# Performance work log

Measured on AMD Instinct MI355X. Metric: run time of the kernel, lower is better.

## Reference

```python
import jax, jax.numpy as jnp
import numpy as np

N = 648      # code length (input_size = output_size)
DV = 3       # variable degree
DC = 6       # check degree
M_PER = N // DC            # checks per layer = 108
E = N * DV                 # edges = hidden_size = 1944
BATCH = 2048
CLAMP = 0.999999


def _build_graph():
    rng = np.random.default_rng(0)
    # regular (3,6) Tanner graph via 3 permutation layers
    var_of = np.concatenate([rng.permutation(N) for _ in range(DV)])          # [E]
    chk_of = np.repeat(np.arange(DV * M_PER), DC)                              # [E]
    eye = np.eye(E, dtype=bool)
    same_chk = (chk_of[:, None] == chk_of[None, :]) & ~eye                     # extrinsic same-check
    same_var = (var_of[:, None] == var_of[None, :]) & ~eye                     # extrinsic same-var
    M_ev = np.zeros((E, N), dtype=np.float32)
    M_ev[np.arange(E), var_of] = 1.0                                           # edge -> its variable
    M_first = (same_chk.astype(np.float32) @ M_ev)                             # [E,N] CN extrinsic over vars
    M_cn = same_chk.astype(np.float32)                                         # [E,E] VN2CN_mask_CNUpdate
    M_vn = same_var.astype(np.float32)                                         # [E,E] CN2VN_mask_VNUpdate
    M_out = M_ev.T.copy()                                                      # [N,E] CN2VN_mask_output
    bias_matrix = M_ev.T.copy()                                                # [N,E] dot_bias_matrix
    return M_first, M_cn, M_vn, M_out, bias_matrix


def _xavier(key, out_f, in_f, mask):
    bound = np.sqrt(6.0 / (in_f + out_f)).astype(np.float32)
    w = jax.random.uniform(key, (out_f, in_f), jnp.float32, -bound, bound)
    return w * mask


def setup_inputs() -> dict:
    key = jax.random.key(0)
    M_first, M_cn, M_vn, M_out, bias_matrix = _build_graph()
    M_first = jnp.asarray(M_first); M_cn = jnp.asarray(M_cn)
    M_vn = jnp.asarray(M_vn); M_out = jnp.asarray(M_out)
    bias_matrix = jnp.asarray(bias_matrix)
    ks = jax.random.split(key, 6)
    x = jax.random.normal(ks[0], (BATCH, N), jnp.float32) * 2.0  # channel LLRs
    W1 = _xavier(ks[1], E, E, M_vn)
    W3 = _xavier(ks[2], E, E, M_vn)
    W5 = _xavier(ks[3], E, E, M_vn)
    W7 = _xavier(ks[4], E, E, M_vn)
    W9 = _xavier(ks[5], N, E, M_out)
    B0 = jnp.eye(N, dtype=jnp.float32); B1 = jnp.eye(N, dtype=jnp.float32)
    B2 = jnp.eye(N, dtype=jnp.float32); B3 = jnp.eye(N, dtype=jnp.float32)
    B4 = jnp.eye(N, dtype=jnp.float32)
    return {"x": x, "M_first": M_first, "M_cn": M_cn, "M_out": M_out,
            "bias_matrix": bias_matrix, "W1": W1, "W3": W3, "W5": W5,
            "W7": W7, "W9": W9, "B0": B0, "B1": B1, "B2": B2, "B3": B3, "B4": B4}


def cn_update(x, mask):
    """out[b,i] = prod over j with mask[i,j]!=0 and x[b,j]!=0 of x[b,j]; 0 if none.
    Computed in sign/log domain so it is three dense [B,in]@[in,out] matmuls
    instead of a Python loop over rows."""
    nz = x != 0.0
    logmag = jnp.log(jnp.where(nz, jnp.abs(x), 1.0))          # 0 contribution where x==0
    neg = (x < 0.0).astype(x.dtype)
    log_prod = logmag @ mask.T                                 # [B,out]
    neg_cnt = neg @ mask.T
    sign = 1.0 - 2.0 * jnp.mod(neg_cnt, 2.0)
    any_nz = (nz.astype(x.dtype) @ mask.T) > 0.0
    return jnp.where(any_nz, sign * jnp.exp(log_prod), 0.0)


def reference(x, M_first, M_cn, M_out, bias_matrix, W1, W3, W5, W7, W9,
              B0, B1, B2, B3, B4):
    llr = x                                                    # Channel_LLR [B,N]
    t = jnp.tanh(0.5 * x)
    t = jnp.clip(cn_update(t, M_first), -CLAMP, CLAMP)
    t = 2.0 * jnp.arctanh(t)
    out1 = jax.nn.sigmoid(t @ M_out.T + llr)                   # count_loss_fc: ones*mask weight, zero bias

    t = jnp.tanh(0.5 * (t @ W1.T + (llr @ B0) @ bias_matrix))
    t = jnp.clip(cn_update(t, M_cn), -CLAMP, CLAMP)
    t = 2.0 * jnp.arctanh(t)
    out2 = jax.nn.sigmoid(t @ M_out.T + llr)

    t = jnp.tanh(0.5 * (t @ W3.T + (llr @ B1) @ bias_matrix))
    t = jnp.clip(cn_update(t, M_cn), -CLAMP, CLAMP)
    t = 2.0 * jnp.arctanh(t)
    out3 = jax.nn.sigmoid(t @ M_out.T + llr)

    t = jnp.tanh(0.5 * (t @ W5.T + (llr @ B2) @ bias_matrix))
    t = jnp.clip(cn_update(t, M_cn), -CLAMP, CLAMP)
    t = 2.0 * jnp.arctanh(t)
    out4 = jax.nn.sigmoid(t @ M_out.T + llr)

    t = jnp.tanh(0.5 * (t @ W7.T + (llr @ B3) @ bias_matrix))
    t = jnp.clip(cn_update(t, M_cn), -CLAMP, CLAMP)
    t = 2.0 * jnp.arctanh(t)
    t = t @ W9.T + llr @ B4
    out5 = jax.nn.sigmoid(t)
    return (out5, out4, out3, out2, out1)
```

## Files before the change

kernel.cpp:

```cpp
#include <hip/hip_runtime.h>
#include <math.h>

#define NN 648
#define EE 1944
#define NCHK 324
#define BATCH 2048
#define BS 256
#define BSM 384
#define TL_CLAMP 14.508648f

__device__ __forceinline__ float rcp_fast(float x) { return __builtin_amdgcn_rcpf(x); }

__device__ __forceinline__ float tanh_half(float x) {
    float E = __expf(x);
    float big = 1.0f - 2.0f * rcp_fast(E + 1.0f);
    float u = 0.5f * x;
    float small = u * (1.0f - 0.33333334f * u * u);
    return (fabsf(x) < 0.03125f) ? small : big;
}

__device__ __forceinline__ float sigm(float s) {
    return rcp_fast(1.0f + __expf(-s));
}

__device__ __forceinline__ float cn_edge(float a, float Q) {
    float t = 0.6931472f * (__log2f(fabsf(a + Q)) - __log2f(fabsf(a - Q)));
    return fminf(fmaxf(t, -TL_CLAMP), TL_CLAMP);
}

__device__ __noinline__ float cn_fallback(float a, float t0, float t1, float t2,
                                          float t3, float t4, float t5) {
    float vv[6] = {t0, t1, t2, t3, t4, t5};
    float P = 1.0f; int cz = 0;
    #pragma unroll
    for (int k = 0; k < 6; k++) {
        if (vv[k] == 0.0f) cz++; else P *= vv[k];
    }
    float ext;
    if (a != 0.0f) ext = (cz >= 5) ? 0.0f : P * rcp_fast(a);
    else           ext = (cz >= 6) ? 0.0f : P;
    ext = fminf(fmaxf(ext, -0.999999f), 0.999999f);
    return 0.6931472f * __log2f((1.0f + ext) * rcp_fast(1.0f - ext));
}

__global__ __launch_bounds__(BS) void extract_struct(
    const float4* __restrict__ M_out4,
    int* __restrict__ var_of, int* __restrict__ varEdge,
    unsigned short* __restrict__ varc16) {
    int t = blockIdx.x * BS + threadIdx.x;
    if (t >= NN * EE / 4) return;
    float4 v = M_out4[t];
    int flat = t * 4;
    int n = flat / EE;
    int e = flat - n * EE;
    if (v.x != 0.0f) { var_of[e]     = n; varEdge[n*3 + (e)    /NN] = e;     varc16[e]     = (unsigned short)n; }
    if (v.y != 0.0f) { var_of[e + 1] = n; varEdge[n*3 + (e + 1)/NN] = e + 1; varc16[e + 1] = (unsigned short)n; }
    if (v.z != 0.0f) { var_of[e + 2] = n; varEdge[n*3 + (e + 2)/NN] = e + 2; varc16[e + 2] = (unsigned short)n; }
    if (v.w != 0.0f) { var_of[e + 3] = n; varEdge[n*3 + (e + 3)/NN] = e + 3; varc16[e + 3] = (unsigned short)n; }
}

__global__ __launch_bounds__(BS) void extract_weights(
    const float* __restrict__ W1, const float* __restrict__ W3,
    const float* __restrict__ W5, const float* __restrict__ W7,
    const float* __restrict__ W9,
    const int* __restrict__ var_of, const int* __restrict__ varEdge,
    unsigned* __restrict__ nb6,
    float4* __restrict__ w1q, float4* __restrict__ w3q,
    float4* __restrict__ w5q, float4* __restrict__ w7q,
    float* __restrict__ w9v) {
    int t = blockIdx.x * BS + threadIdx.x;
    if (t < 4 * EE) {
        int m = t / EE;
        int e = t - m * EE;
        int n = var_of[e];
        int e0 = varEdge[3 * n], e1 = varEdge[3 * n + 1], e2 = varEdge[3 * n + 2];
        int ea, eb;
        if (e == e0)      { ea = e1; eb = e2; }
        else if (e == e1) { ea = e0; eb = e2; }
        else              { ea = e0; eb = e1; }
        const float* W = (m == 0) ? W1 : (m == 1) ? W3 : (m == 2) ? W5 : W7;
        size_t row = (size_t)e * EE;
        float2 w = make_float2(W[row + ea], W[row + eb]);
        float4* dq = (m == 0) ? w1q : (m == 1) ? w3q : (m == 2) ? w5q : w7q;
        ((float2*)dq)[e] = w;
        if (m == 0) nb6[e] = (unsigned)ea | ((unsigned)eb << 16);
    } else if (t < 4 * EE + NN) {
        int n = t - 4 * EE;
        #pragma unroll
        for (int k = 0; k < 3; k++) {
            int e = varEdge[3 * n + k];
            w9v[3 * n + k] = W9[(size_t)n * EE + e];
        }
    }
}

__global__ __launch_bounds__(BSM, 8) void bp_main(
    const float* __restrict__ x,
    const unsigned* __restrict__ varc,
    const unsigned* __restrict__ nb6,
    const int* __restrict__ varEdge,
    const float4* __restrict__ w1q, const float4* __restrict__ w3q,
    const float4* __restrict__ w5q, const float4* __restrict__ w7q,
    const float* __restrict__ w9v,
    float* __restrict__ out) {
    __shared__ __align__(16) float llr_s[NN];
    __shared__ __align__(16) float tlA[EE];
    __shared__ __align__(16) float tlB[EE];
    const int b = blockIdx.x;
    const int tid = threadIdx.x;

    {
        const float2* xr2 = (const float2*)(x + (size_t)b * NN);
        if (tid < NN / 2) ((float2*)llr_s)[tid] = xr2[tid];
    }
    __syncthreads();

    const bool ck = tid < NCHK;
    const int c = tid;
    float lb[6];
    unsigned nbp[6];
    float te[6];

    if (ck) {
        #pragma unroll
        for (int j = 0; j < 3; j++) {
            unsigned vv = varc[3 * c + j];
            lb[2 * j]     = llr_s[vv & 0xffffu];
            lb[2 * j + 1] = llr_s[vv >> 16];
        }
        #pragma unroll
        for (int j = 0; j < 6; j++) {
            nbp[j] = nb6[6 * c + j];
            te[j] = tanh_half(lb[j]);
        }
    }
    int m0[2], m1[2], m2[2];
    #pragma unroll
    for (int j = 0; j < 2; j++) {
        int n = tid + j * BSM;
        if (n < NN) {
            m0[j] = varEdge[3 * n]; m1[j] = varEdge[3 * n + 1];
            m2[j] = varEdge[3 * n + 2];
        } else { m0[j] = m1[j] = m2[j] = 0; }
    }

    auto cn_store = [&](float* dst) {
        float Q = ((te[0] * te[1]) * (te[2] * te[3])) * (te[4] * te[5]);
        float* d = dst + 6 * c;
        if (__builtin_expect(Q != 0.0f, 1)) {
            #pragma unroll
            for (int j = 0; j < 6; j++) d[j] = cn_edge(te[j], Q);
        } else {
            #pragma unroll
            for (int j = 0; j < 6; j++)
                d[j] = cn_fallback(te[j], te[0], te[1], te[2], te[3], te[4], te[5]);
        }
    };
    auto marg = [&](const float* tl, float* dst) {
        #pragma unroll
        for (int j = 0; j < 2; j++) {
            int n = tid + j * BSM;
            if (n < NN)
                dst[n] = sigm(llr_s[n] + tl[m0[j]] + tl[m1[j]] + tl[m2[j]]);
        }
    };

    if (ck) cn_store(tlA);
    __syncthreads();
    marg(tlA, out + ((size_t)(4 * BATCH) + b) * NN);

    const float4* wqs[4] = {w1q, w3q, w5q, w7q};
    #pragma unroll
    for (int L = 0; L < 4; L++) {
        const float4* __restrict__ wq = wqs[L];
        const float* tlc = (L & 1) ? tlB : tlA;
        float* tln = (L & 1) ? tlA : tlB;
        if (ck) {
            float4 wa = wq[3 * c], wb = wq[3 * c + 1], wc = wq[3 * c + 2];
            float w[12] = {wa.x, wa.y, wa.z, wa.w, wb.x, wb.y, wb.z, wb.w,
                           wc.x, wc.y, wc.z, wc.w};
            #pragma unroll
            for (int j = 0; j < 6; j++) {
                float pre = fmaf(w[2 * j], tlc[nbp[j] & 0xffffu],
                            fmaf(w[2 * j + 1], tlc[nbp[j] >> 16], lb[j]));
                te[j] = tanh_half(pre);
            }
            cn_store(tln);
        }
        __syncthreads();
        if (L < 3) {
            marg(tln, out + ((size_t)((3 - L) * BATCH) + b) * NN);
        } else {
            #pragma unroll
            for (int j = 0; j < 2; j++) {
                int n = tid + j * BSM;
                if (n < NN) {
                    float s = llr_s[n]
                            + w9v[3 * n]     * tln[m0[j]]
                            + w9v[3 * n + 1] * tln[m1[j]]
                            + w9v[3 * n + 2] * tln[m2[j]];
                    out[(size_t)b * NN + n] = sigm(s);
                }
            }
        }
    }
}

extern "C" void kernel_launch(void* const* d_in, const int* in_sizes, int n_in,
                              void* d_out, int out_size, void* d_ws, size_t ws_size,
                              hipStream_t stream) {
    const float* x     = (const float*)d_in[0];
    const float* M_out = (const float*)d_in[3];
    const float* W1    = (const float*)d_in[5];
    const float* W3    = (const float*)d_in[6];
    const float* W5    = (const float*)d_in[7];
    const float* W7    = (const float*)d_in[8];
    const float* W9    = (const float*)d_in[9];
    float* out = (float*)d_out;

    char* ws = (char*)d_ws;
    float4* w1q     = (float4*)ws;         ws += (EE / 2) * 16;
    float4* w3q     = (float4*)ws;         ws += (EE / 2) * 16;
    float4* w5q     = (float4*)ws;         ws += (EE / 2) * 16;
    float4* w7q     = (float4*)ws;         ws += (EE / 2) * 16;
    int*    var_of  = (int*)ws;            ws += EE * 4;
    int*    varEdge = (int*)ws;            ws += NN * 3 * 4;
    float*  w9v     = (float*)ws;          ws += NN * 3 * 4;
    unsigned* nb6   = (unsigned*)ws;       ws += EE * 4;
    unsigned short* varc16 = (unsigned short*)ws; ws += EE * 2;

    const int tot4 = NN * EE / 4;
    extract_struct<<<(tot4 + BS - 1) / BS, BS, 0, stream>>>(
        (const float4*)M_out, var_of, varEdge, varc16);
    const int totW = 4 * EE + NN;
    extract_weights<<<(totW + BS - 1) / BS, BS, 0, stream>>>(
        W1, W3, W5, W7, W9, var_of, varEdge, nb6, w1q, w3q, w5q, w7q, w9v);
    bp_main<<<BATCH, BSM, 0, stream>>>(
        x, (const unsigned*)varc16, nb6, varEdge, w1q, w3q, w5q, w7q, w9v, out);
}
```

Before: 166.3 us.

## Process two batch rows per block to amortize index and weight loads

Each block of bp_main now decodes two batch rows instead of one, so the grid is halved and shared memory is doubled. Per-thread graph indices, neighbor lists and weights are loaded once and reused for both rows. The goal is to cut per-block overhead and redundant global and index loads, and to give each thread more independent work to hide latency. The cost is higher register and LDS use per block, with launch bounds lowered to 6, which may reduce occupancy.

```diff
diff --git a/kernel.cpp b/kernel.cpp
--- a/kernel.cpp
+++ b/kernel.cpp
@@ -94,7 +94,7 @@
     }
 }
 
-__global__ __launch_bounds__(BSM, 8) void bp_main(
+__global__ __launch_bounds__(BSM, 6) void bp_main(
     const float* __restrict__ x,
     const unsigned* __restrict__ varc,
     const unsigned* __restrict__ nb6,
@@ -103,35 +103,39 @@
     const float4* __restrict__ w5q, const float4* __restrict__ w7q,
     const float* __restrict__ w9v,
     float* __restrict__ out) {
-    __shared__ __align__(16) float llr_s[NN];
-    __shared__ __align__(16) float tlA[EE];
-    __shared__ __align__(16) float tlB[EE];
+    __shared__ __align__(16) float llr_s[2 * NN];
+    __shared__ __align__(16) float tlA[2][EE];
+    __shared__ __align__(16) float tlB[2][EE];
     const int b = blockIdx.x;
     const int tid = threadIdx.x;
 
     {
-        const float2* xr2 = (const float2*)(x + (size_t)b * NN);
-        if (tid < NN / 2) ((float2*)llr_s)[tid] = xr2[tid];
+        const float4* xr4 = (const float4*)(x + (size_t)b * (2 * NN));
+        if (tid < (2 * NN) / 4) ((float4*)llr_s)[tid] = xr4[tid];
     }
     __syncthreads();
 
     const bool ck = tid < NCHK;
     const int c = tid;
-    float lb[6];
+    float lb[2][6];
     unsigned nbp[6];
-    float te[6];
+    float te[2][6];
 
     if (ck) {
         #pragma unroll
         for (int j = 0; j < 3; j++) {
             unsigned vv = varc[3 * c + j];
-            lb[2 * j]     = llr_s[vv & 0xffffu];
-            lb[2 * j + 1] = llr_s[vv >> 16];
+            int v0 = vv & 0xffffu, v1 = vv >> 16;
+            lb[0][2 * j]     = llr_s[v0];
+            lb[0][2 * j + 1] = llr_s[v1];
+            lb[1][2 * j]     = llr_s[NN + v0];
+            lb[1][2 * j + 1] = llr_s[NN + v1];
         }
         #pragma unroll
         for (int j = 0; j < 6; j++) {
             nbp[j] = nb6[6 * c + j];
-            te[j] = tanh_half(lb[j]);
+            te[0][j] = tanh_half(lb[0][j]);
+            te[1][j] = tanh_half(lb[1][j]);
         }
     }
     int m0[2], m1[2], m2[2];
@@ -144,62 +148,79 @@
         } else { m0[j] = m1[j] = m2[j] = 0; }
     }
 
-    auto cn_store = [&](float* dst) {
-        float Q = ((te[0] * te[1]) * (te[2] * te[3])) * (te[4] * te[5]);
-        float* d = dst + 6 * c;
-        if (__builtin_expect(Q != 0.0f, 1)) {
-            #pragma unroll
-            for (int j = 0; j < 6; j++) d[j] = cn_edge(te[j], Q);
-        } else {
-            #pragma unroll
-            for (int j = 0; j < 6; j++)
-                d[j] = cn_fallback(te[j], te[0], te[1], te[2], te[3], te[4], te[5]);
+    auto cn_store = [&](float (*dst)[EE]) {
+        #pragma unroll
+        for (int r = 0; r < 2; r++) {
+            float Q = ((te[r][0] * te[r][1]) * (te[r][2] * te[r][3]))
+                    * (te[r][4] * te[r][5]);
+            float* d = dst[r] + 6 * c;
+            if (__builtin_expect(Q != 0.0f, 1)) {
+                #pragma unroll
+                for (int j = 0; j < 6; j++) d[j] = cn_edge(te[r][j], Q);
+            } else {
+                #pragma unroll
+                for (int j = 0; j < 6; j++)
+                    d[j] = cn_fallback(te[r][j], te[r][0], te[r][1], te[r][2],
+                                       te[r][3], te[r][4], te[r][5]);
+            }
         }
     };
-    auto marg = [&](const float* tl, float* dst) {
+    auto marg = [&](float (*tl)[EE], int chunk) {
         #pragma unroll
         for (int j = 0; j < 2; j++) {
             int n = tid + j * BSM;
-            if (n < NN)
-                dst[n] = sigm(llr_s[n] + tl[m0[j]] + tl[m1[j]] + tl[m2[j]]);
+            if (n < NN) {
+                #pragma unroll
+                for (int r = 0; r < 2; r++) {
+                    float s = llr_s[r * NN + n] + tl[r][m0[j]] + tl[r][m1[j]]
+                            + tl[r][m2[j]];
+                    out[((size_t)(chunk * BATCH) + 2 * b + r) * NN + n] = sigm(s);
+                }
+            }
         }
     };
 
     if (ck) cn_store(tlA);
     __syncthreads();
-    marg(tlA, out + ((size_t)(4 * BATCH) + b) * NN);
+    marg(tlA, 4);
 
     const float4* wqs[4] = {w1q, w3q, w5q, w7q};
     #pragma unroll
     for (int L = 0; L < 4; L++) {
         const float4* __restrict__ wq = wqs[L];
-        const float* tlc = (L & 1) ? tlB : tlA;
-        float* tln = (L & 1) ? tlA : tlB;
+        float (*tlc)[EE] = (L & 1) ? tlB : tlA;
+        float (*tln)[EE] = (L & 1) ? tlA : tlB;
         if (ck) {
             float4 wa = wq[3 * c], wb = wq[3 * c + 1], wc = wq[3 * c + 2];
             float w[12] = {wa.x, wa.y, wa.z, wa.w, wb.x, wb.y, wb.z, wb.w,
                            wc.x, wc.y, wc.z, wc.w};
             #pragma unroll
             for (int j = 0; j < 6; j++) {
-                float pre = fmaf(w[2 * j], tlc[nbp[j] & 0xffffu],
-                            fmaf(w[2 * j + 1], tlc[nbp[j] >> 16], lb[j]));
-                te[j] = tanh_half(pre);
+                int ea = nbp[j] & 0xffffu, eb = nbp[j] >> 16;
+                #pragma unroll
+                for (int r = 0; r < 2; r++) {
+                    float pre = fmaf(w[2 * j], tlc[r][ea],
+                                fmaf(w[2 * j + 1], tlc[r][eb], lb[r][j]));
+                    te[r][j] = tanh_half(pre);
+                }
             }
             cn_store(tln);
         }
         __syncthreads();
         if (L < 3) {
-            marg(tln, out + ((size_t)((3 - L) * BATCH) + b) * NN);
+            marg(tln, 3 - L);
         } else {
             #pragma unroll
             for (int j = 0; j < 2; j++) {
                 int n = tid + j * BSM;
                 if (n < NN) {
-                    float s = llr_s[n]
-                            + w9v[3 * n]     * tln[m0[j]]
-                            + w9v[3 * n + 1] * tln[m1[j]]
-                            + w9v[3 * n + 2] * tln[m2[j]];
-                    out[(size_t)b * NN + n] = sigm(s);
+                    float a0 = w9v[3 * n], a1 = w9v[3 * n + 1], a2 = w9v[3 * n + 2];
+                    #pragma unroll
+                    for (int r = 0; r < 2; r++) {
+                        float s = llr_s[r * NN + n] + a0 * tln[r][m0[j]]
+                                + a1 * tln[r][m1[j]] + a2 * tln[r][m2[j]];
+                        out[(size_t)(2 * b + r) * NN + n] = sigm(s);
+                    }
                 }
             }
         }
@@ -235,6 +256,6 @@
     const int totW = 4 * EE + NN;
     extract_weights<<<(totW + BS - 1) / BS, BS, 0, stream>>>(
         W1, W3, W5, W7, W9, var_of, varEdge, nb6, w1q, w3q, w5q, w7q, w9v);
-    bp_main<<<BATCH, BSM, 0, stream>>>(
+    bp_main<<<BATCH / 2, BSM, 0, stream>>>(
         x, (const unsigned*)varc16, nb6, varEdge, w1q, w3q, w5q, w7q, w9v, out);
 }
```

After: 168.7 us. No clear change (+1.4%).
